# Kernel optimization log

Measured on AMD Instinct MI355X. Metric: run time of the kernel, lower is better.

## Reference

```python
import jax, jax.numpy as jnp
import numpy as np


def _conv_same(x, w):
    # NHWC input, HWIO kernel, stride 1, SAME padding
    return jax.lax.conv_general_dilated(
        x, w, window_strides=(1, 1), padding='SAME',
        dimension_numbers=('NHWC', 'HWIO', 'NHWC'))


def _maxpool2(x):
    return jax.lax.reduce_window(
        x, -jnp.inf, jax.lax.max,
        window_dimensions=(1, 2, 2, 1), window_strides=(1, 2, 2, 1),
        padding='VALID')


def _binarize(x):
    # sign binarization with straight-through estimator (XNOR-net / Riptide)
    return x + jax.lax.stop_gradient(jnp.sign(x) - x)


def _binary_conv_relu(x, w):
    # BinaryConv2D: binarize activations and weights, conv, relu, no bias
    return jax.nn.relu(_conv_same(_binarize(x), _binarize(w)))


def setup_inputs() -> dict:
    key = jax.random.key(0)
    ks = jax.random.split(key, 32)
    d = {}
    d['x'] = jax.random.normal(ks[0], (128, 32, 32, 3), dtype=jnp.float32)
    d['w1'] = jax.random.normal(ks[1], (3, 3, 3, 128), dtype=jnp.float32) * 0.1
    d['b1'] = jax.random.normal(ks[2], (128,), dtype=jnp.float32) * 0.1
    chans = [128, 128, 256, 256, 512, 512]
    kshapes = [(3, 3, 128, 128), (3, 3, 128, 256), (3, 3, 256, 256),
               (3, 3, 256, 512), (3, 3, 512, 512)]
    for i, shp in zip(range(2, 7), kshapes):
        d[f'w{i}'] = jax.random.normal(ks[2 + i], shp, dtype=jnp.float32) * 0.1
    for i in range(1, 7):
        c = chans[i - 1]
        d[f'bn{i}_scale'] = jax.random.uniform(ks[10 + i], (c,), dtype=jnp.float32, minval=0.5, maxval=1.5)
        d[f'bn{i}_bias'] = jax.random.normal(ks[20 + i], (c,), dtype=jnp.float32) * 0.1
    d['dense_w'] = jax.random.normal(ks[30], (512, 10), dtype=jnp.float32) * 0.05
    d['dense_b'] = jax.random.normal(ks[31], (10,), dtype=jnp.float32) * 0.05
    return d


def reference(x, w1, b1, bn1_scale, bn1_bias, w2, bn2_scale, bn2_bias,
              w3, bn3_scale, bn3_bias, w4, bn4_scale, bn4_bias,
              w5, bn5_scale, bn5_bias, w6, bn6_scale, bn6_bias,
              dense_w, dense_b):
    # conv1: normal float conv + relu, then BN (inference: fused scale/bias)
    h = jax.nn.relu(_conv_same(x, w1) + b1)
    h = h * bn1_scale + bn1_bias
    # conv2 (binary) -> pool -> bn2
    h = _binary_conv_relu(h, w2)
    h = _maxpool2(h)
    h = h * bn2_scale + bn2_bias
    # conv3 (binary) -> bn3
    h = _binary_conv_relu(h, w3)
    h = h * bn3_scale + bn3_bias
    # conv4 (binary) -> pool -> bn4
    h = _binary_conv_relu(h, w4)
    h = _maxpool2(h)
    h = h * bn4_scale + bn4_bias
    # conv5 (binary) -> bn5
    h = _binary_conv_relu(h, w5)
    h = h * bn5_scale + bn5_bias
    # conv6 (binary) -> pool -> bn6
    h = _binary_conv_relu(h, w6)
    h = _maxpool2(h)  # -> [B, 4, 4, 512]
    h = h * bn6_scale + bn6_bias
    # Dense applied on last axis (original code has no flatten): [B,4,4,10]
    logits = jnp.einsum('bhwc,cd->bhwd', h, dense_w) + dense_b
    return jax.nn.softmax(logits, axis=-1)
```

## Files before the change

kernel.cpp:

```cpp
#include <hip/hip_runtime.h>
#include <cstdint>

typedef unsigned long long u64;

__global__ void zero_kernel(u64* __restrict__ p, int n) {
    int i = blockIdx.x * blockDim.x + threadIdx.x;
    int stride = gridDim.x * blockDim.x;
    for (; i < n; i += stride) p[i] = 0;
}

__global__ void pack_weights_kernel(const float* __restrict__ w, u64* __restrict__ wp,
                                    int Cin, int Cout) {
    int tid = blockIdx.x * blockDim.x + threadIdx.x;
    int wid = tid >> 6;
    int lane = threadIdx.x & 63;
    int Wi = Cin >> 6;
    int total = 9 * Wi * Cout;
    if (wid >= total) return;
    int oc = wid % Cout;
    int tw = wid / Cout;
    int tap = tw / Wi;
    int cw = tw % Wi;
    int ci = cw * 64 + lane;
    float v = w[((size_t)tap * Cin + ci) * Cout + oc];
    u64 mask = __ballot(!(v > 0.0f));
    if (lane == 0) wp[(size_t)tw * Cout + oc] = mask;
}

__global__ __launch_bounds__(128) void conv1_pack_kernel(
        const float* __restrict__ x, const float* __restrict__ w1,
        const float* __restrict__ b1, const float* __restrict__ s1,
        const float* __restrict__ bb1, u64* __restrict__ p1) {
    const int t = threadIdx.x;
    const int oc = t;
    const int bx = blockIdx.x;
    const int xseg = (bx & 3) << 3;
    const int y = (bx >> 2) & 31;
    const int b = bx >> 7;

    double wreg[27];
    #pragma unroll
    for (int k = 0; k < 27; k++) wreg[k] = (double)w1[k * 128 + oc];
    const double b1v = (double)b1[oc];
    const double tneg = -(double)bb1[oc] / (double)s1[oc];
    const bool always = tneg < 0.0;
    const double thr = tneg - b1v;

    double acc[8];
    #pragma unroll
    for (int i = 0; i < 8; i++) acc[i] = 0.0;

    #pragma unroll
    for (int ky = 0; ky < 3; ky++) {
        int iy = y - 1 + ky;
        if (iy < 0 || iy > 31) continue;
        #pragma unroll
        for (int col = 0; col < 10; col++) {
            int ix = xseg - 1 + col;
            if (ix < 0 || ix > 31) continue;
            const float* xp = x + ((b * 32 + iy) * 32 + ix) * 3;
            #pragma unroll
            for (int c = 0; c < 3; c++) {
                double xv = (double)xp[c];
                #pragma unroll
                for (int kx = 0; kx < 3; kx++) {
                    int px = col - kx;
                    if (px >= 0 && px < 8)
                        acc[px] += xv * wreg[(ky * 3 + kx) * 3 + c];
                }
            }
        }
    }
    #pragma unroll
    for (int px = 0; px < 8; px++) {
        bool bit = always || (acc[px] > thr);
        u64 m = __ballot(bit);
        if ((t & 63) == 0)
            p1[((size_t)(b * 34 + y + 1) * 34 + xseg + px + 1) * 2 + (t >> 6)] = m;
    }
}

template<int WI, int H, int W, int COUT, bool POOL, int XS, bool BITOUT>
__global__ __launch_bounds__(256, 4) void bconv3_kernel(
        const u64* __restrict__ in, const u64* __restrict__ wp,
        const float* __restrict__ bns, const float* __restrict__ bnb,
        u64* __restrict__ outb, float* __restrict__ outf) {
    constexpr int ROWS = POOL ? 2 : 1;
    constexpr int Ho   = POOL ? H / 2 : H;
    constexpr int Wo   = POOL ? W / 2 : W;
    constexpr int WoW  = COUT >> 6;
    constexpr int Hp   = H + 2, Wp = W + 2;
    constexpr int Wg   = W / XS;
    constexpr int Wog  = Wo / XS;
    constexpr int CH   = (WI < 4) ? WI : 4;
    constexpr int NC   = WI / CH;

    const int lane = threadIdx.x & 63;
    int wid = (blockIdx.x * blockDim.x + threadIdx.x) >> 6;
    wid = __builtin_amdgcn_readfirstlane(wid);
    const int wordo = wid % WoW;
    int t = wid / WoW;
    const int xg = t % XS; t /= XS;
    const int oy = t % Ho;
    const int b  = t / Ho;
    if (b >= 128) return;
    const int oc = wordo * 64 + lane;
    const int c0 = xg * Wg;
    const int base = POOL ? oy * 2 : oy;

    int m[ROWS][Wg];
    #pragma unroll
    for (int r = 0; r < ROWS; r++)
        #pragma unroll
        for (int c = 0; c < Wg; c++) m[r][c] = 0;

    int S_top = 0, S_bot = 0, S_lef = 0, S_rig = 0;
    int C_tl = 0, C_tr = 0, C_bl = 0, C_br = 0;

    const u64* wbase = wp + oc;
    const u64* inb = in + (((size_t)b * Hp + base) * Wp + c0) * WI;

    #pragma unroll 1
    for (int kc = 0; kc < 3 * NC; kc++) {
        const int ky = kc / NC;
        const int ch = kc % NC;
        const int woff = ky * 3 * WI + ch * CH;
        u64 wk[3][CH];
        #pragma unroll
        for (int kx = 0; kx < 3; kx++)
            #pragma unroll
            for (int cw = 0; cw < CH; cw++)
                wk[kx][cw] = wbase[(size_t)(woff + kx * WI + cw) * COUT];

        int pg[3];
        #pragma unroll
        for (int kx = 0; kx < 3; kx++) {
            int s = 0;
            #pragma unroll
            for (int cw = 0; cw < CH; cw++) s += (int)__popcll(wk[kx][cw]);
            pg[kx] = 64 * CH - s;
        }
        S_lef += pg[0]; S_rig += pg[2];
        if (ky == 0) { S_top += pg[0] + pg[1] + pg[2]; C_tl += pg[0]; C_tr += pg[2]; }
        if (ky == 2) { S_bot += pg[0] + pg[1] + pg[2]; C_bl += pg[0]; C_br += pg[2]; }

        #pragma unroll
        for (int r = 0; r < ROWS; r++) {
            const u64* inrow = inb + (size_t)(r + ky) * Wp * WI + ch * CH;
            #pragma unroll
            for (int c = 0; c < Wg + 2; c++) {
                u64 av[CH];
                #pragma unroll
                for (int cw = 0; cw < CH; cw++) av[cw] = inrow[(size_t)c * WI + cw];
                #pragma unroll
                for (int kx = 0; kx < 3; kx++) {
                    const int col = c - kx;
                    if (col < 0 || col >= Wg) continue;
                    int acc = m[r][col];
                    #pragma unroll
                    for (int cw = 0; cw < CH; cw++)
                        acc += (int)__popcll(av[cw] ^ wk[kx][cw]);
                    m[r][col] = acc;
                }
            }
        }
    }

    const double sc = (double)bns[oc];
    const double bi = (double)bnb[oc];

    #pragma unroll
    for (int po = 0; po < Wog; po++) {
        int pmax = 0;
        #pragma unroll
        for (int r = 0; r < ROWS; r++) {
            #pragma unroll
            for (int wx = 0; wx < (POOL ? 2 : 1); wx++) {
                const int lc = POOL ? po * 2 + wx : po;
                const int pc = c0 + lc;
                const int pr = base + r;
                const int top = (pr == 0), bot = (pr == H - 1);
                const int lef = (pc == 0), rig = (pc == W - 1);
                int n_oob = 3 * (top + bot + lef + rig)
                          - (top & lef) - (top & rig) - (bot & lef) - (bot & rig);
                int S = top * S_top + bot * S_bot + lef * S_lef + rig * S_rig
                      - (top & lef) * C_tl - (top & rig) * C_tr
                      - (bot & lef) * C_bl - (bot & rig) * C_br;
                int d = 2 * m[r][lc] + 2 * S - 64 * WI * (9 + n_oob);
                pmax = d > pmax ? d : pmax;
            }
        }
        double h = (double)pmax * sc + bi;
        if constexpr (BITOUT) {
            u64 mask = __ballot(h > 0.0);
            if (lane == 0)
                outb[((size_t)(b * (Ho + 2) + oy + 1) * (Wo + 2) + xg * Wog + po + 1) * WoW + wordo] = mask;
        } else {
            outf[((size_t)(b * Ho + oy) * Wo + xg * Wog + po) * COUT + oc] = (float)h;
        }
    }
}

__global__ __launch_bounds__(256) void dense_softmax_kernel(
        const float* __restrict__ h6, const float* __restrict__ dw,
        const float* __restrict__ db, float* __restrict__ out) {
    int lane = threadIdx.x & 63;
    int r = (blockIdx.x * blockDim.x + threadIdx.x) >> 6;
    if (r >= 2048) return;
    const float* hr = h6 + (size_t)r * 512;
    float part[10];
    #pragma unroll
    for (int d = 0; d < 10; d++) part[d] = 0.f;
    #pragma unroll
    for (int k = 0; k < 8; k++) {
        int c = lane + 64 * k;
        float hv = hr[c];
        const float* dwr = dw + c * 10;
        #pragma unroll
        for (int d = 0; d < 10; d++) part[d] += hv * dwr[d];
    }
    #pragma unroll
    for (int off = 32; off >= 1; off >>= 1) {
        #pragma unroll
        for (int d = 0; d < 10; d++) part[d] += __shfl_down(part[d], off, 64);
    }
    if (lane == 0) {
        float logits[10];
        float mx = -1e30f;
        #pragma unroll
        for (int d = 0; d < 10; d++) { logits[d] = part[d] + db[d]; mx = fmaxf(mx, logits[d]); }
        float se = 0.f;
        #pragma unroll
        for (int d = 0; d < 10; d++) { logits[d] = expf(logits[d] - mx); se += logits[d]; }
        float inv = 1.f / se;
        #pragma unroll
        for (int d = 0; d < 10; d++) out[(size_t)r * 10 + d] = logits[d] * inv;
    }
}

extern "C" void kernel_launch(void* const* d_in, const int* in_sizes, int n_in,
                              void* d_out, int out_size, void* d_ws, size_t ws_size,
                              hipStream_t stream) {
    const float* x    = (const float*)d_in[0];
    const float* w1   = (const float*)d_in[1];
    const float* b1   = (const float*)d_in[2];
    const float* w2   = (const float*)d_in[3];
    const float* w3   = (const float*)d_in[4];
    const float* w4   = (const float*)d_in[5];
    const float* w5   = (const float*)d_in[6];
    const float* w6   = (const float*)d_in[7];
    const float* bn1s = (const float*)d_in[8];
    const float* bn1b = (const float*)d_in[9];
    const float* bn2s = (const float*)d_in[10];
    const float* bn2b = (const float*)d_in[11];
    const float* bn3s = (const float*)d_in[12];
    const float* bn3b = (const float*)d_in[13];
    const float* bn4s = (const float*)d_in[14];
    const float* bn4b = (const float*)d_in[15];
    const float* bn5s = (const float*)d_in[16];
    const float* bn5b = (const float*)d_in[17];
    const float* bn6s = (const float*)d_in[18];
    const float* bn6b = (const float*)d_in[19];
    const float* dw   = (const float*)d_in[20];
    const float* db   = (const float*)d_in[21];
    float* out = (float*)d_out;

    u64* ws  = (u64*)d_ws;
    u64* wp2 = ws;
    u64* wp3 = wp2 + 2304;
    u64* wp4 = wp3 + 4608;
    u64* wp5 = wp4 + 9216;
    u64* wp6 = wp5 + 18432;
    u64* p1  = wp6 + 36864;
    u64* p2  = p1 + 295936;
    u64* p3  = p2 + 82944;
    u64* p4  = p3 + 165888;
    u64* p5  = p4 + 51200;
    float* h6 = (float*)(p5 + 102400);
    const int NPAD = 295936 + 82944 + 165888 + 51200 + 102400;

    zero_kernel<<<1024, 256, 0, stream>>>(p1, NPAD);

    pack_weights_kernel<<<(9*2*128*64)/256, 256, 0, stream>>>(w2, wp2, 128, 128);
    pack_weights_kernel<<<(9*2*256*64)/256, 256, 0, stream>>>(w3, wp3, 128, 256);
    pack_weights_kernel<<<(9*4*256*64)/256, 256, 0, stream>>>(w4, wp4, 256, 256);
    pack_weights_kernel<<<(9*4*512*64)/256, 256, 0, stream>>>(w5, wp5, 256, 512);
    pack_weights_kernel<<<(9*8*512*64)/256, 256, 0, stream>>>(w6, wp6, 512, 512);

    conv1_pack_kernel<<<128*32*4, 128, 0, stream>>>(x, w1, b1, bn1s, bn1b, p1);

    bconv3_kernel<2,32,32,128,true, 2,true ><<<2048, 256, 0, stream>>>(p1, wp2, bn2s, bn2b, p2, nullptr);
    bconv3_kernel<2,16,16,256,false,1,true ><<<2048, 256, 0, stream>>>(p2, wp3, bn3s, bn3b, p3, nullptr);
    bconv3_kernel<4,16,16,256,true, 2,true ><<<2048, 256, 0, stream>>>(p3, wp4, bn4s, bn4b, p4, nullptr);
    bconv3_kernel<4,8,8,512,false,1,true ><<<2048, 256, 0, stream>>>(p4, wp5, bn5s, bn5b, p5, nullptr);
    bconv3_kernel<8,8,8,512,true, 2,false><<<2048, 256, 0, stream>>>(p5, wp6, bn6s, bn6b, nullptr, h6);

    dense_softmax_kernel<<<2048*64/256, 256, 0, stream>>>(h6, dw, db, out);
}
```

Measured before the change: 359.4 us.

## Fuse weight packing with zeroing, transpose packed weights, use chained 32-bit popcounts

Merges the buffer-zeroing kernel and five weight-packing launches into a single prep kernel. Packed binary weights are stored per output channel contiguously, so each lane reads its filter words sequentially instead of with a Cout stride. The XOR-popcount accumulation is written as two 32-bit popcounts chained into the accumulator to map onto the bitcount-with-add instruction. The new layout makes lane loads strided across the wave, which may reduce coalescing in exchange for per-lane contiguity.

```diff
diff --git a/kernel.cpp b/kernel.cpp
--- a/kernel.cpp
+++ b/kernel.cpp
@@ -3,28 +3,44 @@
 
 typedef unsigned long long u64;
 
-__global__ void zero_kernel(u64* __restrict__ p, int n) {
-    int i = blockIdx.x * blockDim.x + threadIdx.x;
-    int stride = gridDim.x * blockDim.x;
-    for (; i < n; i += stride) p[i] = 0;
-}
-
-__global__ void pack_weights_kernel(const float* __restrict__ w, u64* __restrict__ wp,
-                                    int Cin, int Cout) {
-    int tid = blockIdx.x * blockDim.x + threadIdx.x;
-    int wid = tid >> 6;
+__device__ __forceinline__ int pc_acc(u64 a, u64 w, int acc) {
+    u64 x = a ^ w;
+    acc = __builtin_popcount((unsigned)x) + acc;
+    acc = __builtin_popcount((unsigned)(x >> 32)) + acc;
+    return acc;
+}
+
+__global__ __launch_bounds__(256) void prep_kernel(
+        const float* __restrict__ w2, const float* __restrict__ w3,
+        const float* __restrict__ w4, const float* __restrict__ w5,
+        const float* __restrict__ w6,
+        u64* __restrict__ wp2, u64* __restrict__ wp3, u64* __restrict__ wp4,
+        u64* __restrict__ wp5, u64* __restrict__ wp6,
+        u64* __restrict__ pz, int nz) {
+    const int ZB = 1024;
+    if (blockIdx.x < ZB) {
+        int i = blockIdx.x * 256 + threadIdx.x;
+        const int stride = ZB * 256;
+        for (; i < nz; i += stride) pz[i] = 0;
+        return;
+    }
+    int wid = ((blockIdx.x - ZB) * 256 + threadIdx.x) >> 6;
     int lane = threadIdx.x & 63;
-    int Wi = Cin >> 6;
-    int total = 9 * Wi * Cout;
-    if (wid >= total) return;
-    int oc = wid % Cout;
-    int tw = wid / Cout;
-    int tap = tw / Wi;
-    int cw = tw % Wi;
-    int ci = cw * 64 + lane;
-    float v = w[((size_t)tap * Cin + ci) * Cout + oc];
+    const float* w; u64* wp; int Wi, Cout, base;
+    if      (wid <  2304) { w = w2; wp = wp2; Wi = 2; Cout = 128; base = 0; }
+    else if (wid <  6912) { w = w3; wp = wp3; Wi = 2; Cout = 256; base = 2304; }
+    else if (wid < 16128) { w = w4; wp = wp4; Wi = 4; Cout = 256; base = 6912; }
+    else if (wid < 34560) { w = w5; wp = wp5; Wi = 4; Cout = 512; base = 16128; }
+    else if (wid < 71424) { w = w6; wp = wp6; Wi = 8; Cout = 512; base = 34560; }
+    else return;
+    int id = wid - base;
+    int oc = id % Cout;
+    int tw = id / Cout;
+    int tap = tw / Wi, cw = tw % Wi;
+    int Cin = Wi * 64;
+    float v = w[((size_t)tap * Cin + cw * 64 + lane) * Cout + oc];
     u64 mask = __ballot(!(v > 0.0f));
-    if (lane == 0) wp[(size_t)tw * Cout + oc] = mask;
+    if (lane == 0) wp[(size_t)oc * (9 * Wi) + tap * Wi + cw] = mask;
 }
 
 __global__ __launch_bounds__(128) void conv1_pack_kernel(
@@ -81,7 +97,7 @@
 }
 
 template<int WI, int H, int W, int COUT, bool POOL, int XS, bool BITOUT>
-__global__ __launch_bounds__(256, 4) void bconv3_kernel(
+__global__ __launch_bounds__(256, 4) void bconv4_kernel(
         const u64* __restrict__ in, const u64* __restrict__ wp,
         const float* __restrict__ bns, const float* __restrict__ bnb,
         u64* __restrict__ outb, float* __restrict__ outf) {
@@ -117,20 +133,20 @@
     int S_top = 0, S_bot = 0, S_lef = 0, S_rig = 0;
     int C_tl = 0, C_tr = 0, C_bl = 0, C_br = 0;
 
-    const u64* wbase = wp + oc;
+    const u64* wlane = wp + (size_t)oc * (9 * WI);
     const u64* inb = in + (((size_t)b * Hp + base) * Wp + c0) * WI;
 
     #pragma unroll 1
     for (int kc = 0; kc < 3 * NC; kc++) {
         const int ky = kc / NC;
         const int ch = kc % NC;
-        const int woff = ky * 3 * WI + ch * CH;
+        const u64* wptr = wlane + ky * 3 * WI + ch * CH;
         u64 wk[3][CH];
         #pragma unroll
         for (int kx = 0; kx < 3; kx++)
             #pragma unroll
             for (int cw = 0; cw < CH; cw++)
-                wk[kx][cw] = wbase[(size_t)(woff + kx * WI + cw) * COUT];
+                wk[kx][cw] = wptr[kx * WI + cw];
 
         int pg[3];
         #pragma unroll
@@ -159,7 +175,7 @@
                     int acc = m[r][col];
                     #pragma unroll
                     for (int cw = 0; cw < CH; cw++)
-                        acc += (int)__popcll(av[cw] ^ wk[kx][cw]);
+                        acc = pc_acc(av[cw], wk[kx][cw], acc);
                     m[r][col] = acc;
                 }
             }
@@ -279,21 +295,16 @@
     float* h6 = (float*)(p5 + 102400);
     const int NPAD = 295936 + 82944 + 165888 + 51200 + 102400;
 
-    zero_kernel<<<1024, 256, 0, stream>>>(p1, NPAD);
-
-    pack_weights_kernel<<<(9*2*128*64)/256, 256, 0, stream>>>(w2, wp2, 128, 128);
-    pack_weights_kernel<<<(9*2*256*64)/256, 256, 0, stream>>>(w3, wp3, 128, 256);
-    pack_weights_kernel<<<(9*4*256*64)/256, 256, 0, stream>>>(w4, wp4, 256, 256);
-    pack_weights_kernel<<<(9*4*512*64)/256, 256, 0, stream>>>(w5, wp5, 256, 512);
-    pack_weights_kernel<<<(9*8*512*64)/256, 256, 0, stream>>>(w6, wp6, 512, 512);
+    prep_kernel<<<1024 + 17856, 256, 0, stream>>>(
+        w2, w3, w4, w5, w6, wp2, wp3, wp4, wp5, wp6, p1, NPAD);
 
     conv1_pack_kernel<<<128*32*4, 128, 0, stream>>>(x, w1, b1, bn1s, bn1b, p1);
 
-    bconv3_kernel<2,32,32,128,true, 2,true ><<<2048, 256, 0, stream>>>(p1, wp2, bn2s, bn2b, p2, nullptr);
-    bconv3_kernel<2,16,16,256,false,1,true ><<<2048, 256, 0, stream>>>(p2, wp3, bn3s, bn3b, p3, nullptr);
-    bconv3_kernel<4,16,16,256,true, 2,true ><<<2048, 256, 0, stream>>>(p3, wp4, bn4s, bn4b, p4, nullptr);
-    bconv3_kernel<4,8,8,512,false,1,true ><<<2048, 256, 0, stream>>>(p4, wp5, bn5s, bn5b, p5, nullptr);
-    bconv3_kernel<8,8,8,512,true, 2,false><<<2048, 256, 0, stream>>>(p5, wp6, bn6s, bn6b, nullptr, h6);
+    bconv4_kernel<2,32,32,128,true, 2,true ><<<2048, 256, 0, stream>>>(p1, wp2, bn2s, bn2b, p2, nullptr);
+    bconv4_kernel<2,16,16,256,false,1,true ><<<2048, 256, 0, stream>>>(p2, wp3, bn3s, bn3b, p3, nullptr);
+    bconv4_kernel<4,16,16,256,true, 2,true ><<<2048, 256, 0, stream>>>(p3, wp4, bn4s, bn4b, p4, nullptr);
+    bconv4_kernel<4,8,8,512,false,1,true ><<<2048, 256, 0, stream>>>(p4, wp5, bn5s, bn5b, p5, nullptr);
+    bconv4_kernel<8,8,8,512,true, 2,false><<<2048, 256, 0, stream>>>(p5, wp6, bn6s, bn6b, nullptr, h6);
 
     dense_softmax_kernel<<<2048*64/256, 256, 0, stream>>>(h6, dw, db, out);
 }
```

After: 364.2 us. Within noise of the previous version (+1.3%).
